# Kernel tuning notes

Hardware: AMD Instinct MI355X
Metric: run time of the kernel (lower is better)

The kernel has to match this reference:

```python
import jax, jax.numpy as jnp
import numpy as np

B, T, D, K, NF = 4, 1024, 1024, 4, 4
MAXD = 256          # TemporalEncoding max_delta
NC = 32             # ConceptGraph n_concepts
LN_EPS = 1e-5


def setup_inputs() -> dict:
    key = jax.random.key(0)
    ks = jax.random.split(key, 12)
    s = 0.02  # weight init scale
    return {
        "x": jax.random.normal(ks[0], (B, T, D), jnp.float32),
        "routed_tokens": jax.random.normal(ks[1], (B, T, K, D), jnp.float32),
        "sim": jax.random.normal(ks[2], (B, T, K), jnp.float32),
        # per-function logic Linear(3D->D), LayerNorm(D), gate Linear(3D->D)
        "Wl": jax.random.normal(ks[3], (NF, 3 * D, D), jnp.float32) * s,
        "bl": jnp.zeros((NF, D), jnp.float32),
        "ln_g": jnp.ones((NF, D), jnp.float32),
        "ln_b": jnp.zeros((NF, D), jnp.float32),
        "Wg": jax.random.normal(ks[4], (NF, 3 * D, D), jnp.float32) * s,
        "bg": jnp.zeros((NF, D), jnp.float32),
        # fn_selector Linear(D -> NF)
        "Wsel": jax.random.normal(ks[5], (D, NF), jnp.float32) * s,
        "bsel": jnp.zeros((NF,), jnp.float32),
        # temporal embedding table [2*max_delta+1, D]
        "delta_table": jax.random.normal(ks[6], (2 * MAXD + 1, D), jnp.float32) * s,
        # VQ codebook (ConceptGraph.embedding buffer)
        "codebook": jax.random.normal(ks[7], (NC, D), jnp.float32),
        "topk_indices": jax.random.randint(ks[8], (B, T, K), 0, T),
    }


def reference(x, routed_tokens, sim, Wl, bl, ln_g, ln_b, Wg, bg,
              Wsel, bsel, delta_table, codebook, topk_indices):
    Bx, Tx, Dx = x.shape
    Kx = routed_tokens.shape[2]
    N = Bx * Tx

    # temporal encoding: delta = t - topk_index, clamped into table range
    t = jnp.arange(Tx)[None, :, None]
    idx = jnp.clip(t - topk_indices + MAXD, 0, 2 * MAXD)
    de = delta_table[idx].reshape(N, Kx, Dx)            # [N,K,D]

    xf = x.reshape(N, Dx)
    rf = routed_tokens.reshape(N, Kx, Dx)
    sf = sim.reshape(N, Kx)

    tok = jnp.broadcast_to(xf[:, None, :], (N, Kx, Dx))
    comb = jnp.concatenate([tok, rf, de], axis=-1)       # [N,K,3D]

    # all NF reasoning functions at once: logic MLP + GELU + LayerNorm
    h = jnp.einsum('nkc,fcd->fnkd', comb, Wl) + bl[:, None, None, :]
    h = jax.nn.gelu(h, approximate=False)
    mu = jnp.mean(h, axis=-1, keepdims=True)
    var = jnp.var(h, axis=-1, keepdims=True)
    h = (h - mu) / jnp.sqrt(var + LN_EPS)
    h = h * ln_g[:, None, None, :] + ln_b[:, None, None, :]  # [F,N,K,D]

    sw = jax.nn.softmax(sf, axis=-1)                     # [N,K]
    arg = jnp.einsum('nk,fnkd->fnd', sw, h)              # [F,N,D]

    tok_f = jnp.broadcast_to(xf[None], (Wl.shape[0], N, Dx))
    gin = jnp.concatenate([tok_f, arg, arg], axis=-1)    # [F,N,3D]
    gate = jax.nn.sigmoid(jnp.einsum('fnc,fcd->fnd', gin, Wg) + bg[:, None, :])

    fw = jax.nn.softmax(xf @ Wsel + bsel, axis=-1)       # [N,F]
    proposed = jnp.einsum('nf,fnd->nd', fw, arg)
    gsum = jnp.einsum('nf,fnd->nd', fw, gate)
    uf = proposed * gsum                                 # [N,D] updated tokens

    # ConceptGraph VQ (eval: no EMA update): pairwise dist, argmin, gather
    d2 = (jnp.sum(uf * uf, axis=1, keepdims=True)
          - 2.0 * uf @ codebook.T
          + jnp.sum(codebook * codebook, axis=1))        # [N,NC]
    enc = jnp.argmin(d2, axis=1)                         # [N]
    quant = codebook[enc]                                # [N,D]
    out = uf + jax.lax.stop_gradient(quant - uf)         # straight-through
    return out.reshape(Bx, Tx, Dx)
```

## Files before the change

### kernel.cpp

```cpp
#include <hip/hip_runtime.h>
#include <hip/hip_bf16.h>
#include <cmath>


typedef __bf16 bf16x8 __attribute__((ext_vector_type(8)));
typedef float  f32x4  __attribute__((ext_vector_type(4)));

__device__ __forceinline__ float gelu_f(float v) {
    return 0.5f * v * (1.0f + erff(v * 0.7071067811865476f));
}

__device__ __forceinline__ void split8(const float* v, bf16x8& H, bf16x8& L) {
#pragma unroll
    for (int j = 0; j < 8; ++j) {
        float x = v[j];
        __bf16 h = (__bf16)x;
        H[j] = h;
        L[j] = (__bf16)(x - (float)h);
    }
}

#define GLL16(src, dst)                                                        \
    __builtin_amdgcn_global_load_lds(                                          \
        (const __attribute__((address_space(1))) void*)(src),                  \
        (__attribute__((address_space(3))) void*)(dst), 16, 0, 0)

#define SWZ_DECODE()                                                           \
    int bx, by, bz;                                                            \
    {                                                                          \
        const int nx = gridDim.x, ny = gridDim.y;                              \
        const int nwg = nx * ny * (int)gridDim.z;                              \
        const int bid = blockIdx.x + nx * (blockIdx.y + ny * blockIdx.z);      \
        const int q = nwg >> 3;                                                \
        const int rm = (bid & 7) * q + (bid >> 3);                             \
        bx = rm % nx; by = (rm / nx) % ny; bz = rm / (nx * ny);                \
    }

__global__ __launch_bounds__(256) void precvt_img(
    const float* __restrict__ W, char* __restrict__ img,
    int krowBase, int nktLog, int sumFromKt)
{
    const int u = blockIdx.x * 256 + threadIdx.x;
    const int col = u & 127;
    const int kt  = (u >> 7) & ((1 << nktLog) - 1);
    const int ct  = (u >> (7 + nktLog)) & 7;
    const int f   = u >> (10 + nktLog);
    const int colg = ct * 128 + col;
    const float* Wf = W + (size_t)f * 3072 * 1024;
    const bool sum2 = (kt >= sumFromKt);

    float vv[32];
#pragma unroll
    for (int j = 0; j < 32; ++j) {
        int k = krowBase + kt * 32 + j;
        float v = Wf[(size_t)k * 1024 + colg];
        if (sum2) v += Wf[(size_t)(k + 1024) * 1024 + colg];
        vv[j] = v;
    }
    char* tb = img + ((((size_t)f * 8 + ct) << nktLog) + kt) * 16384;
    const int swz = (col >> 1) & 3;
#pragma unroll
    for (int g = 0; g < 4; ++g) {
        bf16x8 H, L; split8(&vv[g * 8], H, L);
        char* dst = tb + col * 64 + ((g ^ swz) << 4);
        *(bf16x8*)dst = H;
        *(bf16x8*)(dst + 8192) = L;
    }
}

#define WRITEA_SPLIT(AB)                                                       \
    {                                                                          \
        int row = tid >> 2, ag = tid & 3;                                      \
        bf16x8 H, L; split8(ra[0], H, L);                                      \
        char* d = (AB) + row * 64 + ((ag ^ ((row >> 1) & 3)) << 4);            \
        *(bf16x8*)d = H; *(bf16x8*)(d + 8192) = L;                             \
        int row2 = row + 64;                                                   \
        split8(ra[1], H, L);                                                   \
        char* d2 = (AB) + row2 * 64 + ((ag ^ ((row2 >> 1) & 3)) << 4);         \
        *(bf16x8*)d2 = H; *(bf16x8*)(d2 + 8192) = L;                           \
    }

#define LOADB_IMG(KT, BB)                                                      \
    {                                                                          \
        const char* sb = Bt + (size_t)(KT) * 16384 + boff;                     \
        char* db = (BB) + boff;                                                \
        GLL16(sb,        db);                                                  \
        GLL16(sb + 1024, db + 1024);                                           \
        GLL16(sb + 2048, db + 2048);                                           \
        GLL16(sb + 3072, db + 3072);                                           \
    }

#define MFMA32(AB, BB)                                                         \
    {                                                                          \
        bf16x8 ah[4], al[4], bh[4], bl_[4];                                    \
        _Pragma("unroll")                                                      \
        for (int mi = 0; mi < 4; ++mi) {                                       \
            const char* pa = (AB) + (wr + mi * 16 + rl) * 64 + goff;           \
            ah[mi] = *(const bf16x8*)pa;                                       \
            al[mi] = *(const bf16x8*)(pa + 8192);                              \
        }                                                                      \
        _Pragma("unroll")                                                      \
        for (int ni = 0; ni < 4; ++ni) {                                       \
            const char* pb = (BB) + (wc + ni * 16 + rl) * 64 + goff;           \
            bh[ni]  = *(const bf16x8*)pb;                                      \
            bl_[ni] = *(const bf16x8*)(pb + 8192);                             \
        }                                                                      \
        _Pragma("unroll")                                                      \
        for (int mi = 0; mi < 4; ++mi)                                         \
            _Pragma("unroll")                                                  \
            for (int ni = 0; ni < 4; ++ni) {                                   \
                acc[mi][ni] = __builtin_amdgcn_mfma_f32_16x16x32_bf16(ah[mi], bh[ni],  acc[mi][ni], 0, 0, 0); \
                acc[mi][ni] = __builtin_amdgcn_mfma_f32_16x16x32_bf16(ah[mi], bl_[ni], acc[mi][ni], 0, 0, 0); \
                acc[mi][ni] = __builtin_amdgcn_mfma_f32_16x16x32_bf16(al[mi], bh[ni],  acc[mi][ni], 0, 0, 0); \
            }                                                                  \
    }

__global__ __launch_bounds__(256, 2) void himg(
    const float* __restrict__ rfA, int rowBase,
    const char* __restrict__ img, int fimg,
    float* __restrict__ hbuf)
{
    __shared__ __align__(16) char lds[65536];
    const int tid = threadIdx.x, wid = tid >> 6, lane = tid & 63;
    SWZ_DECODE();
    (void)bz;
    const int bm0 = bx * 128, bn0 = by * 128;
    const char* Bt = img + (size_t)((fimg * 8 + by) << 5) * 16384;
    const int wr = (wid >> 1) * 64, wc = (wid & 1) * 64;
    const int g = lane >> 4, rl = lane & 15;
    const int goff = ((g ^ ((rl >> 1) & 3)) << 4);
    const int boff = wid * 4096 + lane * 16;
    char* A0 = lds;            char* A1 = lds + 16384;
    char* B0 = lds + 32768;    char* B1 = lds + 49152;

    const float* abase = rfA + (size_t)(rowBase + bm0 + (tid >> 2)) * 1024 + (tid & 3) * 8;
    float ra[2][8];
#define LOADA_H(KT)                                                            \
    {                                                                          \
        const float* s = abase + (KT) * 32;                                    \
        *(float4*)&ra[0][0] = ((const float4*)s)[0];                           \
        *(float4*)&ra[0][4] = ((const float4*)s)[1];                           \
        const float* s2 = s + 64 * 1024;                                       \
        *(float4*)&ra[1][0] = ((const float4*)s2)[0];                          \
        *(float4*)&ra[1][4] = ((const float4*)s2)[1];                          \
    }

    f32x4 acc[4][4];
    f32x4 zero = {0.f, 0.f, 0.f, 0.f};
#pragma unroll
    for (int i = 0; i < 4; ++i)
#pragma unroll
        for (int j = 0; j < 4; ++j) acc[i][j] = zero;

    LOADA_H(0)
    LOADB_IMG(0, B0)
    WRITEA_SPLIT(A0)
    LOADA_H(1)
    __syncthreads();
    for (int kt = 0; kt < 32; ++kt) {
        char* Ac = (kt & 1) ? A1 : A0;  char* Bc = (kt & 1) ? B1 : B0;
        char* An = (kt & 1) ? A0 : A1;  char* Bn = (kt & 1) ? B0 : B1;
        if (kt < 31) {
            LOADB_IMG(kt + 1, Bn)
            WRITEA_SPLIT(An)
            if (kt < 30) LOADA_H(kt + 2)
        }
        MFMA32(Ac, Bc)
        __syncthreads();
    }
#undef LOADA_H

    const int cg = lane & 15, rg = (lane >> 4) * 4;
#pragma unroll
    for (int mi = 0; mi < 4; ++mi)
#pragma unroll
        for (int i = 0; i < 4; ++i) {
            int row_out = bm0 + wr + mi * 16 + rg + i;
#pragma unroll
            for (int ni = 0; ni < 4; ++ni) {
                int col = bn0 + wc + ni * 16 + cg;
                hbuf[(size_t)row_out * 1024 + col] = acc[mi][ni][i];
            }
        }
}

__global__ __launch_bounds__(256, 2) void gate_img(
    const float* __restrict__ x, const float* __restrict__ arg,
    const char* __restrict__ img, const float* __restrict__ fw,
    const float* __restrict__ bg, float* __restrict__ g2, int fbase)
{
    __shared__ __align__(16) char lds[65536];
    const int tid = threadIdx.x, wid = tid >> 6, lane = tid & 63;
    SWZ_DECODE();
    const int bm0 = bx * 128, bn0 = by * 128;
    const int z = bz, f = fbase + z;
    const float* argf = arg + (size_t)f * 4096 * 1024;
    const char* Bt = img + (size_t)((f * 8 + by) << 6) * 16384;
    const int wr = (wid >> 1) * 64, wc = (wid & 1) * 64;
    const int g = lane >> 4, rl = lane & 15;
    const int goff = ((g ^ ((rl >> 1) & 3)) << 4);
    const int boff = wid * 4096 + lane * 16;
    char* A0 = lds;            char* A1 = lds + 16384;
    char* B0 = lds + 32768;    char* B1 = lds + 49152;

    const int arow = bm0 + (tid >> 2);
    const int akc  = (tid & 3) * 8;
    float ra[2][8];
#define LOADA_G(KT)                                                            \
    {                                                                          \
        int k0 = (KT) * 32 + akc;                                              \
        const float* base = (k0 < 1024) ? x : (argf - 1024);                   \
        const float* s  = base + (size_t)arow * 1024 + k0;                     \
        const float* s2 = base + (size_t)(arow + 64) * 1024 + k0;              \
        *(float4*)&ra[0][0] = ((const float4*)s)[0];                           \
        *(float4*)&ra[0][4] = ((const float4*)s)[1];                           \
        *(float4*)&ra[1][0] = ((const float4*)s2)[0];                          \
        *(float4*)&ra[1][4] = ((const float4*)s2)[1];                          \
    }

    f32x4 acc[4][4];
    f32x4 zero = {0.f, 0.f, 0.f, 0.f};
#pragma unroll
    for (int i = 0; i < 4; ++i)
#pragma unroll
        for (int j = 0; j < 4; ++j) acc[i][j] = zero;

    LOADA_G(0)
    LOADB_IMG(0, B0)
    WRITEA_SPLIT(A0)
    LOADA_G(1)
    __syncthreads();
    for (int kt = 0; kt < 64; ++kt) {
        char* Ac = (kt & 1) ? A1 : A0;  char* Bc = (kt & 1) ? B1 : B0;
        char* An = (kt & 1) ? A0 : A1;  char* Bn = (kt & 1) ? B0 : B1;
        if (kt < 63) {
            LOADB_IMG(kt + 1, Bn)
            WRITEA_SPLIT(An)
            if (kt < 62) LOADA_G(kt + 2)
        }
        MFMA32(Ac, Bc)
        __syncthreads();
    }
#undef LOADA_G

    const int cg = lane & 15, rg = (lane >> 4) * 4;
    const bool accum = (fbase > 0);
#pragma unroll
    for (int mi = 0; mi < 4; ++mi)
#pragma unroll
        for (int i = 0; i < 4; ++i) {
            int row_out = bm0 + wr + mi * 16 + rg + i;
            float fwv = fw[(size_t)row_out * 4 + f];
#pragma unroll
            for (int ni = 0; ni < 4; ++ni) {
                int col = bn0 + wc + ni * 16 + cg;
                float v = acc[mi][ni][i] + bg[f * 1024 + col];
                float s = fwv / (1.0f + expf(-v));
                size_t off = ((size_t)z * 4096 + row_out) * 1024 + col;
                if (accum) g2[off] += s; else g2[off] = s;
            }
        }
}

#define STAGE_WRITE64()                                                        \
    _Pragma("unroll")                                                          \
    for (int i = 0; i < 4; ++i) {                                              \
        int u = tid + i * 256;                                                 \
        int arow = u >> 3, ag = u & 7;                                         \
        bf16x8 H, L; split8(rav[i], H, L);                                     \
        char* dst = lds + arow * 128 + ((ag ^ (arow & 7)) << 4);               \
        *(bf16x8*)dst = H; *(bf16x8*)(dst + 16384) = L;                        \
    }                                                                          \
    _Pragma("unroll")                                                          \
    for (int i = 0; i < 4; ++i) {                                              \
        int u = tid + i * 256;                                                 \
        int bcol = u & 127, bgu = u >> 7;                                      \
        bf16x8 H, L; split8(rbv[i], H, L);                                     \
        char* dst = lds + 32768 + bcol * 128 + ((bgu ^ (bcol & 7)) << 4);      \
        *(bf16x8*)dst = H; *(bf16x8*)(dst + 16384) = L;                        \
    }

#define MFMA64()                                                               \
    _Pragma("unroll")                                                          \
    for (int ks = 0; ks < 2; ++ks) {                                           \
        bf16x8 ah[4], al[4], bh[4], bl_[4];                                    \
        _Pragma("unroll")                                                      \
        for (int mi = 0; mi < 4; ++mi) {                                       \
            const char* pa = lds + (wr + mi * 16 + rl) * 128                   \
                             + (((ks * 4 + g) ^ (rl & 7)) << 4);               \
            ah[mi] = *(const bf16x8*)pa;                                       \
            al[mi] = *(const bf16x8*)(pa + 16384);                             \
        }                                                                      \
        _Pragma("unroll")                                                      \
        for (int ni = 0; ni < 4; ++ni) {                                       \
            const char* pb = lds + 32768 + (wc + ni * 16 + rl) * 128           \
                             + (((ks * 4 + g) ^ (rl & 7)) << 4);               \
            bh[ni]  = *(const bf16x8*)pb;                                      \
            bl_[ni] = *(const bf16x8*)(pb + 16384);                            \
        }                                                                      \
        _Pragma("unroll")                                                      \
        for (int mi = 0; mi < 4; ++mi)                                         \
            _Pragma("unroll")                                                  \
            for (int ni = 0; ni < 4; ++ni) {                                   \
                acc[mi][ni] = __builtin_amdgcn_mfma_f32_16x16x32_bf16(ah[mi], bh[ni],  acc[mi][ni], 0, 0, 0); \
                acc[mi][ni] = __builtin_amdgcn_mfma_f32_16x16x32_bf16(ah[mi], bl_[ni], acc[mi][ni], 0, 0, 0); \
                acc[mi][ni] = __builtin_amdgcn_mfma_f32_16x16x32_bf16(al[mi], bh[ni],  acc[mi][ni], 0, 0, 0); \
            }                                                                  \
    }

__global__ __launch_bounds__(256, 2) void gemm64(
    const float* __restrict__ A, int arowBase, int maxrow,
    const float* __restrict__ B, int kbase,
    float* __restrict__ C, int nkt,
    size_t bStrideZ, size_t cStrideZ, int mrows)
{
    __shared__ __align__(16) char lds[65536];
    const int tid = threadIdx.x, wid = tid >> 6, lane = tid & 63;
    SWZ_DECODE();
    const int bm0 = bx * 128, bn0 = by * 128;
    const float* Bf = B + bz * bStrideZ;
    float* Cp = C + bz * cStrideZ;
    const int wr = (wid >> 1) * 64, wc = (wid & 1) * 64;
    const int g = lane >> 4, rl = lane & 15;

    float rav[4][8], rbv[4][8];

#define LOADA64(KC0)                                                           \
    _Pragma("unroll")                                                          \
    for (int i = 0; i < 4; ++i) {                                              \
        int u = tid + i * 256;                                                 \
        int r = arowBase + bm0 + (u >> 3); if (r > maxrow) r = maxrow;         \
        const float* s = A + (size_t)r * 1024 + (KC0) + (u & 7) * 8;           \
        *(float4*)&rav[i][0] = ((const float4*)s)[0];                          \
        *(float4*)&rav[i][4] = ((const float4*)s)[1];                          \
    }
#define LOADB64(KC0)                                                           \
    _Pragma("unroll")                                                          \
    for (int i = 0; i < 4; ++i) {                                              \
        int u = tid + i * 256;                                                 \
        int bcol = bn0 + (u & 127);                                            \
        int k0 = kbase + (KC0) + (u >> 7) * 8;                                 \
        _Pragma("unroll")                                                      \
        for (int j = 0; j < 8; ++j)                                            \
            rbv[i][j] = Bf[(size_t)(k0 + j) * 1024 + bcol];                    \
    }

    f32x4 acc[4][4];
    f32x4 zero = {0.f, 0.f, 0.f, 0.f};
#pragma unroll
    for (int i = 0; i < 4; ++i)
#pragma unroll
        for (int j = 0; j < 4; ++j) acc[i][j] = zero;

    LOADA64(0) LOADB64(0)
    for (int kt = 0; kt < nkt; ++kt) {
        STAGE_WRITE64()
        __syncthreads();
        if (kt + 1 < nkt) { LOADA64((kt + 1) * 64) LOADB64((kt + 1) * 64) }
        MFMA64()
        __syncthreads();
    }
#undef LOADA64
#undef LOADB64

    const int cg = lane & 15, rg = (lane >> 4) * 4;
#pragma unroll
    for (int mi = 0; mi < 4; ++mi)
#pragma unroll
        for (int i = 0; i < 4; ++i) {
            int row_out = bm0 + wr + mi * 16 + rg + i;
            if (row_out >= mrows) continue;
#pragma unroll
            for (int ni = 0; ni < 4; ++ni) {
                int col = bn0 + wc + ni * 16 + cg;
                Cp[(size_t)row_out * 1024 + col] = acc[mi][ni][i];
            }
        }
}

__global__ __launch_bounds__(256) void fw_kernel(
    const float* __restrict__ x, const float* __restrict__ Wsel,
    const float* __restrict__ bsel, float* __restrict__ fw)
{
    __shared__ float sred[16];
    const int n = blockIdx.x;
    const int tid = threadIdx.x, w = tid >> 6, lane = tid & 63;

    float4 xv = *(const float4*)&x[(size_t)n * 1024 + tid * 4];
    float pf0 = 0, pf1 = 0, pf2 = 0, pf3 = 0;
    const float* wrp = &Wsel[(size_t)tid * 16];
    pf0 += xv.x * wrp[0];  pf1 += xv.x * wrp[1];  pf2 += xv.x * wrp[2];  pf3 += xv.x * wrp[3];
    pf0 += xv.y * wrp[4];  pf1 += xv.y * wrp[5];  pf2 += xv.y * wrp[6];  pf3 += xv.y * wrp[7];
    pf0 += xv.z * wrp[8];  pf1 += xv.z * wrp[9];  pf2 += xv.z * wrp[10]; pf3 += xv.z * wrp[11];
    pf0 += xv.w * wrp[12]; pf1 += xv.w * wrp[13]; pf2 += xv.w * wrp[14]; pf3 += xv.w * wrp[15];
    for (int o = 32; o; o >>= 1) {
        pf0 += __shfl_xor(pf0, o); pf1 += __shfl_xor(pf1, o);
        pf2 += __shfl_xor(pf2, o); pf3 += __shfl_xor(pf3, o);
    }
    if (lane == 0) { sred[w*4+0] = pf0; sred[w*4+1] = pf1; sred[w*4+2] = pf2; sred[w*4+3] = pf3; }
    __syncthreads();
    if (tid == 0) {
        float s0 = sred[0] + sred[4] + sred[8]  + sred[12] + bsel[0];
        float s1 = sred[1] + sred[5] + sred[9]  + sred[13] + bsel[1];
        float s2 = sred[2] + sred[6] + sred[10] + sred[14] + bsel[2];
        float s3 = sred[3] + sred[7] + sred[11] + sred[15] + bsel[3];
        float mx = fmaxf(fmaxf(s0, s1), fmaxf(s2, s3));
        float e0 = expf(s0 - mx), e1 = expf(s1 - mx), e2 = expf(s2 - mx), e3 = expf(s3 - mx);
        float inv = 1.0f / (e0 + e1 + e2 + e3);
        float4 o = { e0 * inv, e1 * inv, e2 * inv, e3 * inv };
        *(float4*)&fw[(size_t)n * 4] = o;
    }
}

__global__ __launch_bounds__(256) void ln_fuse_kernel(
    const float* __restrict__ hpre, const float* __restrict__ de_proj,
    const float* __restrict__ bl, const float* __restrict__ ln_g,
    const float* __restrict__ ln_b, const float* __restrict__ sim,
    const int* __restrict__ topk, float* arg,
    int f, int token_base, const float* xl)
{
    __shared__ float red[4 * 1024];
    const int n = token_base + blockIdx.x;
    const int k = threadIdx.x >> 6, lane = threadIdx.x & 63;
    const float* hrow = hpre + ((size_t)blockIdx.x * 4 + k) * 1024;
    const int t  = n & 1023;
    const int tk = topk[(size_t)n * 4 + k];
    int di = t - tk + 256; di = di < 0 ? 0 : (di > 512 ? 512 : di);
    const float* drow = de_proj + ((size_t)f * 513 + di) * 1024;
    const float* blr = bl + f * 1024;
    const float* gr  = ln_g + f * 1024;
    const float* br  = ln_b + f * 1024;
    const float* xr  = xl + (size_t)n * 1024;

    float4 s4 = *(const float4*)&sim[(size_t)n * 4];
    float smax = fmaxf(fmaxf(s4.x, s4.y), fmaxf(s4.z, s4.w));
    float e0 = expf(s4.x - smax), e1 = expf(s4.y - smax);
    float e2 = expf(s4.z - smax), e3 = expf(s4.w - smax);
    float swk = (k == 0 ? e0 : k == 1 ? e1 : k == 2 ? e2 : e3) / (e0 + e1 + e2 + e3);

    float gv[16];
    float ssum = 0.f;
#pragma unroll
    for (int j = 0; j < 4; ++j) {
        int d4 = lane + j * 64;
        float4 h  = *(const float4*)&hrow[d4 * 4];
        float4 dd = *(const float4*)&drow[d4 * 4];
        float4 bb = *(const float4*)&blr[d4 * 4];
        float4 xv = *(const float4*)&xr[d4 * 4];
        float a0 = gelu_f(h.x + xv.x + dd.x + bb.x);
        float a1 = gelu_f(h.y + xv.y + dd.y + bb.y);
        float a2 = gelu_f(h.z + xv.z + dd.z + bb.z);
        float a3 = gelu_f(h.w + xv.w + dd.w + bb.w);
        gv[j*4+0] = a0; gv[j*4+1] = a1; gv[j*4+2] = a2; gv[j*4+3] = a3;
        ssum += a0 + a1 + a2 + a3;
    }
    for (int o = 32; o; o >>= 1) ssum += __shfl_xor(ssum, o);
    float mu = ssum * 0.0009765625f;
    float vs = 0.f;
#pragma unroll
    for (int i = 0; i < 16; ++i) { float dm = gv[i] - mu; vs += dm * dm; }
    for (int o = 32; o; o >>= 1) vs += __shfl_xor(vs, o);
    float rstd = 1.0f / sqrtf(vs * 0.0009765625f + 1e-5f);
#pragma unroll
    for (int j = 0; j < 4; ++j) {
        int d4 = lane + j * 64;
        float4 g4 = *(const float4*)&gr[d4 * 4];
        float4 b4 = *(const float4*)&br[d4 * 4];
        float4 y;
        y.x = ((gv[j*4+0] - mu) * rstd * g4.x + b4.x) * swk;
        y.y = ((gv[j*4+1] - mu) * rstd * g4.y + b4.y) * swk;
        y.z = ((gv[j*4+2] - mu) * rstd * g4.z + b4.z) * swk;
        y.w = ((gv[j*4+3] - mu) * rstd * g4.w + b4.w) * swk;
        *(float4*)&red[k * 1024 + d4 * 4] = y;
    }
    __syncthreads();
    const int p = threadIdx.x;
    float4 r0 = *(const float4*)&red[0 * 1024 + p * 4];
    float4 r1 = *(const float4*)&red[1 * 1024 + p * 4];
    float4 r2 = *(const float4*)&red[2 * 1024 + p * 4];
    float4 r3 = *(const float4*)&red[3 * 1024 + p * 4];
    float4 o;
    o.x = r0.x + r1.x + r2.x + r3.x;
    o.y = r0.y + r1.y + r2.y + r3.y;
    o.z = r0.z + r1.z + r2.z + r3.z;
    o.w = r0.w + r1.w + r2.w + r3.w;
    *(float4*)&arg[((size_t)f * 4096 + n) * 1024 + p * 4] = o;
}

__global__ __launch_bounds__(256) void final_kernel(
    const float* __restrict__ fw, const float* __restrict__ arg,
    const float* __restrict__ g2, const float* __restrict__ cb,
    float* __restrict__ out)
{
    __shared__ float uf_s[1024];
    __shared__ float score_s[32];
    __shared__ int enc_s;
    const int n = blockIdx.x;
    const int tid = threadIdx.x, w = tid >> 6, lane = tid & 63;

    float4 fwv = *(const float4*)&fw[(size_t)n * 4];
    float fwa[4] = { fwv.x, fwv.y, fwv.z, fwv.w };

    float4 prop = {0, 0, 0, 0};
#pragma unroll
    for (int f = 0; f < 4; ++f) {
        float4 av = *(const float4*)&arg[((size_t)f * 4096 + n) * 1024 + tid * 4];
        prop.x += fwa[f] * av.x; prop.y += fwa[f] * av.y;
        prop.z += fwa[f] * av.z; prop.w += fwa[f] * av.w;
    }
    float4 ga = *(const float4*)&g2[(size_t)n * 1024 + tid * 4];
    float4 gb = *(const float4*)&g2[(size_t)(4096 + n) * 1024 + tid * 4];
    float4 uf;
    uf.x = prop.x * (ga.x + gb.x); uf.y = prop.y * (ga.y + gb.y);
    uf.z = prop.z * (ga.z + gb.z); uf.w = prop.w * (ga.w + gb.w);
    *(float4*)&uf_s[tid * 4] = uf;
    __syncthreads();

#pragma unroll
    for (int cc = 0; cc < 8; ++cc) {
        int c = w * 8 + cc;
        float p = 0.f, q = 0.f;
#pragma unroll
        for (int j = 0; j < 4; ++j) {
            int d4 = lane + j * 64;
            float4 u4 = *(const float4*)&uf_s[d4 * 4];
            float4 c4 = *(const float4*)&cb[(size_t)c * 1024 + d4 * 4];
            p += u4.x * c4.x + u4.y * c4.y + u4.z * c4.z + u4.w * c4.w;
            q += c4.x * c4.x + c4.y * c4.y + c4.z * c4.z + c4.w * c4.w;
        }
        float s = q - 2.0f * p;
        for (int o = 32; o; o >>= 1) s += __shfl_xor(s, o);
        if (lane == 0) score_s[c] = s;
    }
    __syncthreads();
    if (tid < 64) {
        float v; int idx;
        if (lane < 32) { v = score_s[lane]; idx = lane; }
        else           { v = INFINITY;      idx = 1 << 30; }
        for (int o = 16; o; o >>= 1) {
            float ov = __shfl_xor(v, o); int oi = __shfl_xor(idx, o);
            if (ov < v || (ov == v && oi < idx)) { v = ov; idx = oi; }
        }
        if (lane == 0) enc_s = idx;
    }
    __syncthreads();
    const int enc = enc_s;
    float4 o4 = *(const float4*)&cb[(size_t)enc * 1024 + tid * 4];
    *(float4*)&out[(size_t)n * 1024 + tid * 4] = o4;
}

extern "C" void kernel_launch(void* const* d_in, const int* in_sizes, int n_in,
                              void* d_out, int out_size, void* d_ws, size_t ws_size,
                              hipStream_t stream)
{
    const float* x    = (const float*)d_in[0];
    const float* rf   = (const float*)d_in[1];
    const float* sim  = (const float*)d_in[2];
    const float* Wl   = (const float*)d_in[3];
    const float* bl   = (const float*)d_in[4];
    const float* ln_g = (const float*)d_in[5];
    const float* ln_b = (const float*)d_in[6];
    const float* Wg   = (const float*)d_in[7];
    const float* bg   = (const float*)d_in[8];
    const float* Wsel = (const float*)d_in[9];
    const float* bsel = (const float*)d_in[10];
    const float* dtab = (const float*)d_in[11];
    const float* cb   = (const float*)d_in[12];
    const int*   topk = (const int*)d_in[13];
    float* out = (float*)d_out;
    dim3 blk(256);

    const size_t NEED = 142622720ull;
    if (ws_size < NEED) return;
    char* ws = (char*)d_ws;
    float* arg     = (float*)(ws + 0);
    float* de_proj = (float*)(ws + 67108864);
    float* hbuf    = (float*)(ws + 75513856);
    char*  Wl1img  = ws + 109068288;
    char*  Wgimg   = ws + 67108864;
    float* g2      = (float*)(ws + 100663296);
    float* fw      = (float*)(ws + 134217728);

    gemm64<<<dim3(5, 8, 4), blk, 0, stream>>>(
        dtab, 0, 512, Wl, 2048, de_proj, 16,
        (size_t)3072 * 1024, (size_t)513 * 1024, 513);

    gemm64<<<dim3(32, 8, 4), blk, 0, stream>>>(
        x, 0, 4095, Wl, 0, arg, 16,
        (size_t)3072 * 1024, (size_t)4096 * 1024, 4096);

    precvt_img<<<512, blk, 0, stream>>>(Wl, Wl1img, 1024, 5, 99);

    for (int f = 0; f < 4; ++f) {
        const float* xlf = arg + (size_t)f * 4096 * 1024;
        for (int ch = 0; ch < 2; ++ch) {
            himg<<<dim3(64, 8), blk, 0, stream>>>(
                rf, ch * 8192, Wl1img, f, hbuf);
            ln_fuse_kernel<<<2048, blk, 0, stream>>>(
                hbuf, de_proj, bl, ln_g, ln_b, sim, topk, arg,
                f, ch * 2048, xlf);
        }
    }

    precvt_img<<<1024, blk, 0, stream>>>(Wg, Wgimg, 0, 6, 32);

    fw_kernel<<<4096, blk, 0, stream>>>(x, Wsel, bsel, fw);

    gate_img<<<dim3(32, 8, 2), blk, 0, stream>>>(x, arg, Wgimg, fw, bg, g2, 0);
    gate_img<<<dim3(32, 8, 2), blk, 0, stream>>>(x, arg, Wgimg, fw, bg, g2, 2);

    final_kernel<<<4096, blk, 0, stream>>>(fw, arg, g2, cb, out);
}
```

Measured before the change: 1.012 ms.

## Split-K the delta-table projection and route x projection through pre-converted image GEMM

The small delta-table projection (513 rows) launched only 160 blocks with a 16-step K loop. It is now split four ways along K into 640 blocks, followed by a reduce kernel, to fill the GPU better. The x-token projection moves from the generic gemm64, which splits fp32 into bf16 hi/lo in registers each tile, to the img-based GEMM kernel. That kernel reads a pre-converted Wl slice written by an added precvt_img pass. This costs an extra weight-conversion pass, extra partial-sum traffic and another workspace region.

```diff
diff --git a/kernel.cpp b/kernel.cpp
--- a/kernel.cpp
+++ b/kernel.cpp
@@ -115,17 +115,18 @@
             }                                                                  \
     }
 
-__global__ __launch_bounds__(256, 2) void himg(
-    const float* __restrict__ rfA, int rowBase,
-    const char* __restrict__ img, int fimg,
-    float* __restrict__ hbuf)
+__global__ __launch_bounds__(256, 2) void gemm_img(
+    const float* __restrict__ A, int rowBase,
+    const char* __restrict__ img, int fimgBase,
+    float* __restrict__ C, size_t cStrideZ)
 {
     __shared__ __align__(16) char lds[65536];
     const int tid = threadIdx.x, wid = tid >> 6, lane = tid & 63;
     SWZ_DECODE();
-    (void)bz;
     const int bm0 = bx * 128, bn0 = by * 128;
+    const int fimg = fimgBase + bz;
     const char* Bt = img + (size_t)((fimg * 8 + by) << 5) * 16384;
+    float* Cp = C + (size_t)bz * cStrideZ;
     const int wr = (wid >> 1) * 64, wc = (wid & 1) * 64;
     const int g = lane >> 4, rl = lane & 15;
     const int goff = ((g ^ ((rl >> 1) & 3)) << 4);
@@ -133,7 +134,7 @@
     char* A0 = lds;            char* A1 = lds + 16384;
     char* B0 = lds + 32768;    char* B1 = lds + 49152;
 
-    const float* abase = rfA + (size_t)(rowBase + bm0 + (tid >> 2)) * 1024 + (tid & 3) * 8;
+    const float* abase = A + (size_t)(rowBase + bm0 + (tid >> 2)) * 1024 + (tid & 3) * 8;
     float ra[2][8];
 #define LOADA_H(KT)                                                            \
     {                                                                          \
@@ -179,7 +180,7 @@
 #pragma unroll
             for (int ni = 0; ni < 4; ++ni) {
                 int col = bn0 + wc + ni * 16 + cg;
-                hbuf[(size_t)row_out * 1024 + col] = acc[mi][ni][i];
+                Cp[(size_t)row_out * 1024 + col] = acc[mi][ni][i];
             }
         }
 }
@@ -282,19 +283,19 @@
 
 #define MFMA64()                                                               \
     _Pragma("unroll")                                                          \
-    for (int ks = 0; ks < 2; ++ks) {                                           \
+    for (int ks2 = 0; ks2 < 2; ++ks2) {                                        \
         bf16x8 ah[4], al[4], bh[4], bl_[4];                                    \
         _Pragma("unroll")                                                      \
         for (int mi = 0; mi < 4; ++mi) {                                       \
             const char* pa = lds + (wr + mi * 16 + rl) * 128                   \
-                             + (((ks * 4 + g) ^ (rl & 7)) << 4);               \
+                             + (((ks2 * 4 + g) ^ (rl & 7)) << 4);              \
             ah[mi] = *(const bf16x8*)pa;                                       \
             al[mi] = *(const bf16x8*)(pa + 16384);                             \
         }                                                                      \
         _Pragma("unroll")                                                      \
         for (int ni = 0; ni < 4; ++ni) {                                       \
             const char* pb = lds + 32768 + (wc + ni * 16 + rl) * 128           \
-                             + (((ks * 4 + g) ^ (rl & 7)) << 4);               \
+                             + (((ks2 * 4 + g) ^ (rl & 7)) << 4);              \
             bh[ni]  = *(const bf16x8*)pb;                                      \
             bl_[ni] = *(const bf16x8*)(pb + 16384);                            \
         }                                                                      \
@@ -308,38 +309,38 @@
             }                                                                  \
     }
 
-__global__ __launch_bounds__(256, 2) void gemm64(
-    const float* __restrict__ A, int arowBase, int maxrow,
-    const float* __restrict__ B, int kbase,
-    float* __restrict__ C, int nkt,
-    size_t bStrideZ, size_t cStrideZ, int mrows)
+__global__ __launch_bounds__(256, 2) void deproj_part(
+    const float* __restrict__ dtab, const float* __restrict__ Wl,
+    float* __restrict__ pbase)
 {
     __shared__ __align__(16) char lds[65536];
     const int tid = threadIdx.x, wid = tid >> 6, lane = tid & 63;
     SWZ_DECODE();
     const int bm0 = bx * 128, bn0 = by * 128;
-    const float* Bf = B + bz * bStrideZ;
-    float* Cp = C + bz * cStrideZ;
+    const int f = bz & 3, ks = bz >> 2;
+    const int akb = ks * 256;
+    const float* Bf = Wl + (size_t)f * 3072 * 1024 + (size_t)(2048 + ks * 256) * 1024;
+    float* Cp = pbase + (size_t)ks * 2101248 + (size_t)f * 525312;
     const int wr = (wid >> 1) * 64, wc = (wid & 1) * 64;
     const int g = lane >> 4, rl = lane & 15;
 
     float rav[4][8], rbv[4][8];
 
-#define LOADA64(KC0)                                                           \
+#define LOADA_D(KC0)                                                           \
     _Pragma("unroll")                                                          \
     for (int i = 0; i < 4; ++i) {                                              \
         int u = tid + i * 256;                                                 \
-        int r = arowBase + bm0 + (u >> 3); if (r > maxrow) r = maxrow;         \
-        const float* s = A + (size_t)r * 1024 + (KC0) + (u & 7) * 8;           \
+        int r = bm0 + (u >> 3); if (r > 512) r = 512;                          \
+        const float* s = dtab + (size_t)r * 1024 + akb + (KC0) + (u & 7) * 8;  \
         *(float4*)&rav[i][0] = ((const float4*)s)[0];                          \
         *(float4*)&rav[i][4] = ((const float4*)s)[1];                          \
     }
-#define LOADB64(KC0)                                                           \
+#define LOADB_D(KC0)                                                           \
     _Pragma("unroll")                                                          \
     for (int i = 0; i < 4; ++i) {                                              \
         int u = tid + i * 256;                                                 \
         int bcol = bn0 + (u & 127);                                            \
-        int k0 = kbase + (KC0) + (u >> 7) * 8;                                 \
+        int k0 = (KC0) + (u >> 7) * 8;                                         \
         _Pragma("unroll")                                                      \
         for (int j = 0; j < 8; ++j)                                            \
             rbv[i][j] = Bf[(size_t)(k0 + j) * 1024 + bcol];                    \
@@ -352,16 +353,16 @@
 #pragma unroll
         for (int j = 0; j < 4; ++j) acc[i][j] = zero;
 
-    LOADA64(0) LOADB64(0)
-    for (int kt = 0; kt < nkt; ++kt) {
+    LOADA_D(0) LOADB_D(0)
+    for (int kt = 0; kt < 4; ++kt) {
         STAGE_WRITE64()
         __syncthreads();
-        if (kt + 1 < nkt) { LOADA64((kt + 1) * 64) LOADB64((kt + 1) * 64) }
+        if (kt + 1 < 4) { LOADA_D((kt + 1) * 64) LOADB_D((kt + 1) * 64) }
         MFMA64()
         __syncthreads();
     }
-#undef LOADA64
-#undef LOADB64
+#undef LOADA_D
+#undef LOADB_D
 
     const int cg = lane & 15, rg = (lane >> 4) * 4;
 #pragma unroll
@@ -369,13 +370,27 @@
 #pragma unroll
         for (int i = 0; i < 4; ++i) {
             int row_out = bm0 + wr + mi * 16 + rg + i;
-            if (row_out >= mrows) continue;
+            if (row_out >= 513) continue;
 #pragma unroll
             for (int ni = 0; ni < 4; ++ni) {
                 int col = bn0 + wc + ni * 16 + cg;
                 Cp[(size_t)row_out * 1024 + col] = acc[mi][ni][i];
             }
         }
+}
+
+__global__ __launch_bounds__(256) void deproj_reduce(float* __restrict__ p)
+{
+    const size_t i = ((size_t)blockIdx.x * 256 + threadIdx.x) * 4;
+    float4 a = *(float4*)&p[i];
+    float4 b = *(const float4*)&p[i + 2101248];
+    float4 c = *(const float4*)&p[i + 4202496];
+    float4 d = *(const float4*)&p[i + 6303744];
+    a.x = ((a.x + b.x) + c.x) + d.x;
+    a.y = ((a.y + b.y) + c.y) + d.y;
+    a.z = ((a.z + b.z) + c.z) + d.z;
+    a.w = ((a.w + b.w) + c.w) + d.w;
+    *(float4*)&p[i] = a;
 }
 
 __global__ __launch_bounds__(256) void fw_kernel(
@@ -577,25 +592,25 @@
     float* de_proj = (float*)(ws + 67108864);
     float* hbuf    = (float*)(ws + 75513856);
     char*  Wl1img  = ws + 109068288;
+    char*  Wl0img  = ws + 125845504;
     char*  Wgimg   = ws + 67108864;
     float* g2      = (float*)(ws + 100663296);
     float* fw      = (float*)(ws + 134217728);
 
-    gemm64<<<dim3(5, 8, 4), blk, 0, stream>>>(
-        dtab, 0, 512, Wl, 2048, de_proj, 16,
-        (size_t)3072 * 1024, (size_t)513 * 1024, 513);
-
-    gemm64<<<dim3(32, 8, 4), blk, 0, stream>>>(
-        x, 0, 4095, Wl, 0, arg, 16,
-        (size_t)3072 * 1024, (size_t)4096 * 1024, 4096);
+    deproj_part<<<dim3(5, 8, 16), blk, 0, stream>>>(dtab, Wl, de_proj);
+    deproj_reduce<<<2052, blk, 0, stream>>>(de_proj);
+
+    precvt_img<<<512, blk, 0, stream>>>(Wl, Wl0img, 0, 5, 99);
+    gemm_img<<<dim3(32, 8, 4), blk, 0, stream>>>(
+        x, 0, Wl0img, 0, arg, (size_t)4096 * 1024);
 
     precvt_img<<<512, blk, 0, stream>>>(Wl, Wl1img, 1024, 5, 99);
 
     for (int f = 0; f < 4; ++f) {
         const float* xlf = arg + (size_t)f * 4096 * 1024;
         for (int ch = 0; ch < 2; ++ch) {
-            himg<<<dim3(64, 8), blk, 0, stream>>>(
-                rf, ch * 8192, Wl1img, f, hbuf);
+            gemm_img<<<dim3(64, 8, 1), blk, 0, stream>>>(
+                rf, ch * 8192, Wl1img, f, hbuf, 0);
             ln_fuse_kernel<<<2048, blk, 0, stream>>>(
                 hbuf, de_proj, bl, ln_g, ln_b, sim, topk, arg,
                 f, ch * 2048, xlf);
```

Result: no change. 994.7 us (-1.7%).
